# Kernel optimization log

Hardware: AMD Instinct MI355X
Metric: run time of the kernel (lower is better)

Reference implementation:

```python
import jax, jax.numpy as jnp
import numpy as np

N = 4096
IN_F = 256
OUT_F = 64
K = 4
ALPHA = 0.2  # LeakyReLU negative slope
NEG_INF = -9e15


def setup_inputs() -> dict:
    key = jax.random.key(0)
    k_h, k_w, k_a, k_e, k_m = jax.random.split(key, 5)
    h = jax.random.normal(k_h, (N, IN_F), dtype=jnp.float32)
    # xavier_uniform with gain=1.414
    def xavier(k, shape, gain=1.414):
        fan_in, fan_out = shape[0], shape[1]
        limit = gain * np.sqrt(6.0 / (fan_in + fan_out))
        return jax.random.uniform(k, shape, jnp.float32, -limit, limit)
    W = xavier(k_w, (IN_F, OUT_F))
    a = xavier(k_a, (2 * OUT_F, 1))
    vals = jax.random.uniform(k_e, (K, N, N), dtype=jnp.float32)
    mask = jax.random.uniform(k_m, (K, N, N), dtype=jnp.float32) < 0.05
    edge_attr = jnp.where(mask, vals, 0.0)
    return {"h": h, "edge_attr": edge_attr, "W": W, "a": a}


def reference(h, edge_attr, W, a):
    # h: [N, IN_F], edge_attr: [K, N, N], W: [IN_F, OUT_F], a: [2*OUT_F, 1]
    Wh = h @ W                                   # [N, OUT_F]
    Wh1 = Wh @ a[:OUT_F, :]                      # [N, 1]
    Wh2 = Wh @ a[OUT_F:, :]                      # [N, 1]
    e = jax.nn.leaky_relu(Wh1 + Wh2.T, negative_slope=ALPHA)  # [N, N]
    e = e[None, :, :] * edge_attr                # [K, N, N]
    e = jnp.where(edge_attr > 0, e, NEG_INF)
    att = jax.nn.softmax(e, axis=1)              # softmax over dim=1, as in torch
    # dropout is identity in eval mode
    # batched replacement for the per-channel python loop of matmuls
    hp = jnp.einsum('kij,jf->kif', att, Wh)      # [K, N, OUT_F]
    out = jnp.transpose(hp, (1, 0, 2)).reshape(N, K * OUT_F)  # concat dim=1
    return jax.nn.elu(out), att
```

## Files before the change

### kernel.cpp

```cpp
#include <hip/hip_runtime.h>

#define NN 4096
#define IN_F 256
#define OUT_F 64
#define K_CH 4
#define ALPHA 0.2f
#define JP 16
#define JCOLS 256
#define ROWS1 8
#define IC1 512

typedef __bf16 bf16;
typedef __attribute__((ext_vector_type(8))) __bf16 bf16x8;
typedef __attribute__((ext_vector_type(4))) float f32x4;

__global__ __launch_bounds__(256) void k0_wh(const float* __restrict__ h,
                                             const float* __restrict__ W,
                                             const float* __restrict__ a,
                                             float* __restrict__ Wh,
                                             float* __restrict__ Wh1,
                                             float* __restrict__ Wh2) {
    int tid = threadIdx.x;
    int wave = tid >> 6, lane = tid & 63;
    int i = blockIdx.x * 4 + wave;
    const float* hrow = h + (size_t)i * IN_F;
    float acc = 0.f;
    #pragma unroll 8
    for (int c = 0; c < IN_F; ++c)
        acc += hrow[c] * W[c * OUT_F + lane];
    Wh[(size_t)i * OUT_F + lane] = acc;
    float v1 = acc * a[lane];
    float v2 = acc * a[OUT_F + lane];
    #pragma unroll
    for (int o = 32; o > 0; o >>= 1) {
        v1 += __shfl_xor(v1, o, 64);
        v2 += __shfl_xor(v2, o, 64);
    }
    if (lane == 0) { Wh1[i] = v1; Wh2[i] = v2; }
}

__global__ __launch_bounds__(256) void k0_transpose(const float* __restrict__ Wh,
                                                    bf16* __restrict__ WhT) {
    __shared__ float lds[OUT_F * 65];
    int tid = threadIdx.x;
    int i0 = blockIdx.x * 64;
    int f = tid & 63;
    int r0 = tid >> 6;
    #pragma unroll
    for (int s = 0; s < 16; ++s) {
        int r = r0 * 16 + s;
        lds[f * 65 + r] = Wh[(size_t)(i0 + r) * OUT_F + f];
    }
    __syncthreads();
    int f2 = tid >> 2;
    int c0 = (tid & 3) * 16;
    #pragma unroll
    for (int s = 0; s < 16; ++s) {
        int c = c0 + s;
        WhT[(size_t)f2 * NN + i0 + c] = (bf16)lds[f2 * 65 + c];
    }
}

__global__ __launch_bounds__(256) void k1_colsum(const float* __restrict__ edge_ch,
                                                 const float* __restrict__ Wh1,
                                                 const float* __restrict__ Wh2,
                                                 float* __restrict__ partial) {
    int tid = threadIdx.x;
    int j0 = blockIdx.y * 2048 + tid * 8;
    int ic = blockIdx.x;
    int ibase = ic * ROWS1;
    float w2[8];
    {
        f32x4 t0 = *(const f32x4*)&Wh2[j0];
        f32x4 t1 = *(const f32x4*)&Wh2[j0 + 4];
        #pragma unroll
        for (int c = 0; c < 4; ++c) { w2[c] = t0[c]; w2[c + 4] = t1[c]; }
    }
    float s[8] = {0.f, 0.f, 0.f, 0.f, 0.f, 0.f, 0.f, 0.f};
    const float* base = edge_ch + (size_t)ibase * NN + j0;
    f32x4 r0[4], r1[4];
    #pragma unroll
    for (int t = 0; t < 4; ++t) {
        r0[t] = *(const f32x4*)(base + (size_t)t * NN);
        r1[t] = *(const f32x4*)(base + (size_t)t * NN + 4);
    }
    #pragma unroll
    for (int ii = 0; ii < ROWS1; ++ii) {
        int cur = ii & 3;
        f32x4 e0 = r0[cur], e1 = r1[cur];
        int ip = (ii + 4 < ROWS1) ? ii + 4 : ii;
        r0[cur] = *(const f32x4*)(base + (size_t)ip * NN);
        r1[cur] = *(const f32x4*)(base + (size_t)ip * NN + 4);
        float wh1 = Wh1[ibase + ii];
        #pragma unroll
        for (int c = 0; c < 8; ++c) {
            float ef = c < 4 ? e0[c] : e1[c - 4];
            float xv = wh1 + w2[c];
            float lk = xv > 0.f ? xv : ALPHA * xv;
            s[c] += ef > 0.f ? __expf(lk * ef) : 0.f;
        }
    }
    float* pr = partial + (size_t)ic * NN + j0;
    f32x4 o0, o1;
    #pragma unroll
    for (int c = 0; c < 4; ++c) { o0[c] = s[c]; o1[c] = s[c + 4]; }
    *(f32x4*)pr = o0;
    *(f32x4*)(pr + 4) = o1;
}

__global__ __launch_bounds__(256) void k1_reduce(const float* __restrict__ partial,
                                                 float* __restrict__ s_col) {
    __shared__ float red[256];
    int tid = threadIdx.x;
    int jl = tid & 63, g = tid >> 6;
    int j = blockIdx.x * 64 + jl;
    float s = 0.f;
    #pragma unroll 8
    for (int t = 0; t < IC1 / 4; ++t)
        s += partial[(size_t)(g * (IC1 / 4) + t) * NN + j];
    red[tid] = s;
    __syncthreads();
    if (tid < 64)
        s_col[j] = red[tid] + red[tid + 64] + red[tid + 128] + red[tid + 192];
}

__global__ __launch_bounds__(256) void k2_fused(const float* __restrict__ edge_ch,
                                                const float* __restrict__ Wh1,
                                                const float* __restrict__ Wh2,
                                                const float* __restrict__ s_col,
                                                const bf16* __restrict__ WhT,
                                                float* __restrict__ att_ch,
                                                float* __restrict__ hp) {
    __shared__ float lds_inv[JCOLS];
    __shared__ float lds_w2[JCOLS];
    int tid = threadIdx.x;
    int itile = blockIdx.x;
    int jp = blockIdx.y;
    int jbase0 = jp * JCOLS;
    {
        float s0 = s_col[jbase0 + tid];
        lds_inv[tid] = s0 > 0.f ? 1.f / s0 : 0.f;
        lds_w2[tid]  = Wh2[jbase0 + tid];
    }
    __syncthreads();
    int wave = tid >> 6, lane = tid & 63;
    int n16 = lane & 15, quad = lane >> 4;
    int i_row = itile * 64 + wave * 16 + n16;
    float wh1 = Wh1[i_row];
    const size_t ebase = (size_t)i_row * NN + jbase0 + quad * 8;
    const float* eptr = edge_ch + ebase;
    float* aptr = att_ch + ebase;
    const bf16* wbase = WhT + (size_t)n16 * NN + jbase0 + quad * 8;
    f32x4 acc[4] = {};
    f32x4 p0[4], p1[4];
    #pragma unroll
    for (int t = 0; t < 4; ++t) {
        p0[t] = *(const f32x4*)(eptr + t * 32);
        p1[t] = *(const f32x4*)(eptr + t * 32 + 4);
    }
    #pragma unroll
    for (int s = 0; s < JCOLS / 32; ++s) {
        int cur = s & 3;
        f32x4 e0 = p0[cur], e1 = p1[cur];
        int sp = (s + 4 < JCOLS / 32) ? s + 4 : s;
        p0[cur] = *(const f32x4*)(eptr + sp * 32);
        p1[cur] = *(const f32x4*)(eptr + sp * 32 + 4);
        int jl = s * 32 + quad * 8;
        f32x4 iv0 = *(const f32x4*)&lds_inv[jl];
        f32x4 iv1 = *(const f32x4*)&lds_inv[jl + 4];
        f32x4 wv0 = *(const f32x4*)&lds_w2[jl];
        f32x4 wv1 = *(const f32x4*)&lds_w2[jl + 4];
        bf16x8 afrag;
        f32x4 av0, av1;
        #pragma unroll
        for (int c = 0; c < 8; ++c) {
            float ef = c < 4 ? e0[c] : e1[c - 4];
            float w2c = c < 4 ? wv0[c] : wv1[c - 4];
            float isc = c < 4 ? iv0[c] : iv1[c - 4];
            float xv = wh1 + w2c;
            float lk = xv > 0.f ? xv : ALPHA * xv;
            float attv = ef > 0.f ? __expf(lk * ef) * isc : 0.f;
            afrag[c] = (bf16)attv;
            if (c < 4) av0[c] = attv; else av1[c - 4] = attv;
        }
        __builtin_nontemporal_store(av0, (f32x4*)(aptr + s * 32));
        __builtin_nontemporal_store(av1, (f32x4*)(aptr + s * 32 + 4));
        #pragma unroll
        for (int ft = 0; ft < 4; ++ft) {
            bf16x8 bfrag = *(const bf16x8*)(wbase + (size_t)ft * 16 * NN + s * 32);
            acc[ft] = __builtin_amdgcn_mfma_f32_16x16x32_bf16(afrag, bfrag, acc[ft], 0, 0, 0);
        }
    }
    #pragma unroll
    for (int ft = 0; ft < 4; ++ft) {
        #pragma unroll
        for (int r = 0; r < 4; ++r) {
            int row_l = quad * 4 + r;
            int i_g = itile * 64 + wave * 16 + row_l;
            size_t idx = ((size_t)jp * NN + i_g) * OUT_F + ft * 16 + n16;
            hp[idx] = acc[ft][r];
        }
    }
}

__global__ __launch_bounds__(256) void k3_combine(const float* __restrict__ hp,
                                                  float* __restrict__ out,
                                                  int kch) {
    int g = blockIdx.x * 256 + threadIdx.x;
    int i = g >> 6;
    int f = g & 63;
    float s = 0.f;
    #pragma unroll
    for (int z = 0; z < JP; ++z)
        s += hp[((size_t)z * NN + i) * OUT_F + f];
    out[(size_t)i * (K_CH * OUT_F) + kch * OUT_F + f] = s > 0.f ? s : __expf(s) - 1.f;
}

extern "C" void kernel_launch(void* const* d_in, const int* in_sizes, int n_in,
                              void* d_out, int out_size, void* d_ws, size_t ws_size,
                              hipStream_t stream) {
    (void)out_size; (void)ws_size;
    const float *h = nullptr, *edge = nullptr, *W = nullptr, *a = nullptr;
    for (int i = 0; i < n_in; ++i) {
        int sz = in_sizes[i];
        if (sz == NN * IN_F)               h    = (const float*)d_in[i];
        else if (sz == K_CH * NN * NN)     edge = (const float*)d_in[i];
        else if (sz == IN_F * OUT_F)       W    = (const float*)d_in[i];
        else if (sz == 2 * OUT_F)          a    = (const float*)d_in[i];
    }

    char* ws = (char*)d_ws;
    float* Wh      = (float*)(ws);
    float* Wh1     = (float*)(ws + 1048576);
    float* Wh2     = (float*)(ws + 1048576 + 16384);
    float* s_col   = (float*)(ws + 1048576 + 32768);
    bf16*  WhT     = (bf16*) (ws + 1048576 + 49152);
    float* partial = (float*)(ws + 1048576 + 49152 + 524288);
    float* hp      = (float*)(ws + 1048576 + 49152 + 524288 + 8388608);

    float* out_h   = (float*)d_out;
    float* att_out = out_h + (size_t)NN * (K_CH * OUT_F);

    k0_wh<<<dim3(NN / 4), 256, 0, stream>>>(h, W, a, Wh, Wh1, Wh2);
    k0_transpose<<<dim3(NN / 64), 256, 0, stream>>>(Wh, WhT);

    for (int ch = 0; ch < K_CH; ++ch) {
        const float* edge_ch = edge + (size_t)ch * NN * NN;
        float* att_ch = att_out + (size_t)ch * NN * NN;
        k1_colsum<<<dim3(IC1, 2), 256, 0, stream>>>(edge_ch, Wh1, Wh2, partial);
        k1_reduce<<<dim3(NN / 64), 256, 0, stream>>>(partial, s_col);
        k2_fused<<<dim3(64, JP), 256, 0, stream>>>(edge_ch, Wh1, Wh2, s_col, WhT, att_ch, hp);
        k3_combine<<<dim3(NN * OUT_F / 256), 256, 0, stream>>>(hp, out_h, ch);
    }
}
```

Before: 628.6 us.

## Materialize bf16 exp values in colsum pass and reuse them in attention kernel

```diff
diff --git a/kernel.cpp b/kernel.cpp
--- a/kernel.cpp
+++ b/kernel.cpp
@@ -5,10 +5,10 @@
 #define OUT_F 64
 #define K_CH 4
 #define ALPHA 0.2f
-#define JP 16
-#define JCOLS 256
-#define ROWS1 8
-#define IC1 512
+#define JP 8
+#define JCOLS 512
+#define ROWS1 16
+#define IC1 256
 
 typedef __bf16 bf16;
 typedef __attribute__((ext_vector_type(8))) __bf16 bf16x8;
@@ -64,6 +64,7 @@
 __global__ __launch_bounds__(256) void k1_colsum(const float* __restrict__ edge_ch,
                                                  const float* __restrict__ Wh1,
                                                  const float* __restrict__ Wh2,
+                                                 bf16* __restrict__ p_ch,
                                                  float* __restrict__ partial) {
     int tid = threadIdx.x;
     int j0 = blockIdx.y * 2048 + tid * 8;
@@ -78,13 +79,14 @@
     }
     float s[8] = {0.f, 0.f, 0.f, 0.f, 0.f, 0.f, 0.f, 0.f};
     const float* base = edge_ch + (size_t)ibase * NN + j0;
+    bf16* pbase = p_ch + (size_t)ibase * NN + j0;
     f32x4 r0[4], r1[4];
     #pragma unroll
     for (int t = 0; t < 4; ++t) {
         r0[t] = *(const f32x4*)(base + (size_t)t * NN);
         r1[t] = *(const f32x4*)(base + (size_t)t * NN + 4);
     }
-    #pragma unroll
+    #pragma unroll 4
     for (int ii = 0; ii < ROWS1; ++ii) {
         int cur = ii & 3;
         f32x4 e0 = r0[cur], e1 = r1[cur];
@@ -92,13 +94,18 @@
         r0[cur] = *(const f32x4*)(base + (size_t)ip * NN);
         r1[cur] = *(const f32x4*)(base + (size_t)ip * NN + 4);
         float wh1 = Wh1[ibase + ii];
+        bf16x8 pv;
         #pragma unroll
         for (int c = 0; c < 8; ++c) {
             float ef = c < 4 ? e0[c] : e1[c - 4];
             float xv = wh1 + w2[c];
             float lk = xv > 0.f ? xv : ALPHA * xv;
-            s[c] += ef > 0.f ? __expf(lk * ef) : 0.f;
-        }
+            float val = ef > 0.f ? __expf(lk * ef) : 0.f;
+            bf16 vb = (bf16)val;
+            pv[c] = vb;
+            s[c] += (float)vb;
+        }
+        *(bf16x8*)(pbase + (size_t)ii * NN) = pv;
     }
     float* pr = partial + (size_t)ic * NN + j0;
     f32x4 o0, o1;
@@ -124,62 +131,51 @@
         s_col[j] = red[tid] + red[tid + 64] + red[tid + 128] + red[tid + 192];
 }
 
-__global__ __launch_bounds__(256) void k2_fused(const float* __restrict__ edge_ch,
-                                                const float* __restrict__ Wh1,
-                                                const float* __restrict__ Wh2,
+__global__ __launch_bounds__(256) void k2_fused(const bf16* __restrict__ p_ch,
                                                 const float* __restrict__ s_col,
                                                 const bf16* __restrict__ WhT,
                                                 float* __restrict__ att_ch,
                                                 float* __restrict__ hp) {
     __shared__ float lds_inv[JCOLS];
-    __shared__ float lds_w2[JCOLS];
     int tid = threadIdx.x;
     int itile = blockIdx.x;
     int jp = blockIdx.y;
     int jbase0 = jp * JCOLS;
     {
-        float s0 = s_col[jbase0 + tid];
-        lds_inv[tid] = s0 > 0.f ? 1.f / s0 : 0.f;
-        lds_w2[tid]  = Wh2[jbase0 + tid];
+        int t2 = tid * 2;
+        float s0 = s_col[jbase0 + t2];
+        float s1 = s_col[jbase0 + t2 + 1];
+        lds_inv[t2]     = s0 > 0.f ? 1.f / s0 : 0.f;
+        lds_inv[t2 + 1] = s1 > 0.f ? 1.f / s1 : 0.f;
     }
     __syncthreads();
     int wave = tid >> 6, lane = tid & 63;
     int n16 = lane & 15, quad = lane >> 4;
     int i_row = itile * 64 + wave * 16 + n16;
-    float wh1 = Wh1[i_row];
     const size_t ebase = (size_t)i_row * NN + jbase0 + quad * 8;
-    const float* eptr = edge_ch + ebase;
+    const bf16* pptr = p_ch + ebase;
     float* aptr = att_ch + ebase;
     const bf16* wbase = WhT + (size_t)n16 * NN + jbase0 + quad * 8;
     f32x4 acc[4] = {};
-    f32x4 p0[4], p1[4];
-    #pragma unroll
-    for (int t = 0; t < 4; ++t) {
-        p0[t] = *(const f32x4*)(eptr + t * 32);
-        p1[t] = *(const f32x4*)(eptr + t * 32 + 4);
-    }
-    #pragma unroll
+    bf16x8 pf[4];
+    #pragma unroll
+    for (int t = 0; t < 4; ++t)
+        pf[t] = *(const bf16x8*)(pptr + t * 32);
+    #pragma unroll 4
     for (int s = 0; s < JCOLS / 32; ++s) {
         int cur = s & 3;
-        f32x4 e0 = p0[cur], e1 = p1[cur];
+        bf16x8 pv = pf[cur];
         int sp = (s + 4 < JCOLS / 32) ? s + 4 : s;
-        p0[cur] = *(const f32x4*)(eptr + sp * 32);
-        p1[cur] = *(const f32x4*)(eptr + sp * 32 + 4);
+        pf[cur] = *(const bf16x8*)(pptr + sp * 32);
         int jl = s * 32 + quad * 8;
         f32x4 iv0 = *(const f32x4*)&lds_inv[jl];
         f32x4 iv1 = *(const f32x4*)&lds_inv[jl + 4];
-        f32x4 wv0 = *(const f32x4*)&lds_w2[jl];
-        f32x4 wv1 = *(const f32x4*)&lds_w2[jl + 4];
         bf16x8 afrag;
         f32x4 av0, av1;
         #pragma unroll
         for (int c = 0; c < 8; ++c) {
-            float ef = c < 4 ? e0[c] : e1[c - 4];
-            float w2c = c < 4 ? wv0[c] : wv1[c - 4];
             float isc = c < 4 ? iv0[c] : iv1[c - 4];
-            float xv = wh1 + w2c;
-            float lk = xv > 0.f ? xv : ALPHA * xv;
-            float attv = ef > 0.f ? __expf(lk * ef) * isc : 0.f;
+            float attv = (float)pv[c] * isc;
             afrag[c] = (bf16)attv;
             if (c < 4) av0[c] = attv; else av1[c - 4] = attv;
         }
@@ -230,13 +226,15 @@
     }
 
     char* ws = (char*)d_ws;
-    float* Wh      = (float*)(ws);
-    float* Wh1     = (float*)(ws + 1048576);
-    float* Wh2     = (float*)(ws + 1048576 + 16384);
-    float* s_col   = (float*)(ws + 1048576 + 32768);
-    bf16*  WhT     = (bf16*) (ws + 1048576 + 49152);
-    float* partial = (float*)(ws + 1048576 + 49152 + 524288);
-    float* hp      = (float*)(ws + 1048576 + 49152 + 524288 + 8388608);
+    size_t off = 0;
+    float* Wh      = (float*)(ws + off); off += (size_t)NN * OUT_F * 4;
+    float* Wh1     = (float*)(ws + off); off += NN * 4;
+    float* Wh2     = (float*)(ws + off); off += NN * 4;
+    float* s_col   = (float*)(ws + off); off += NN * 4;
+    bf16*  WhT     = (bf16*) (ws + off); off += (size_t)OUT_F * NN * 2;
+    float* partial = (float*)(ws + off); off += (size_t)IC1 * NN * 4;
+    float* hp      = (float*)(ws + off); off += (size_t)JP * NN * OUT_F * 4;
+    bf16*  p_buf   = (bf16*) (ws + off); off += (size_t)NN * NN * 2;
 
     float* out_h   = (float*)d_out;
     float* att_out = out_h + (size_t)NN * (K_CH * OUT_F);
@@ -247,9 +245,9 @@
     for (int ch = 0; ch < K_CH; ++ch) {
         const float* edge_ch = edge + (size_t)ch * NN * NN;
         float* att_ch = att_out + (size_t)ch * NN * NN;
-        k1_colsum<<<dim3(IC1, 2), 256, 0, stream>>>(edge_ch, Wh1, Wh2, partial);
+        k1_colsum<<<dim3(IC1, 2), 256, 0, stream>>>(edge_ch, Wh1, Wh2, p_buf, partial);
         k1_reduce<<<dim3(NN / 64), 256, 0, stream>>>(partial, s_col);
-        k2_fused<<<dim3(64, JP), 256, 0, stream>>>(edge_ch, Wh1, Wh2, s_col, WhT, att_ch, hp);
+        k2_fused<<<dim3(64, JP), 256, 0, stream>>>(p_buf, s_col, WhT, att_ch, hp);
         k3_combine<<<dim3(NN * OUT_F / 256), 256, 0, stream>>>(hp, out_h, ch);
     }
 }
```

Result: slower. 644.6 us (+2.6%).
